# Kernel optimization log

Measured on AMD Instinct MI355X. Metric: run time of the kernel, lower is better.

The kernel has to match this reference:

```python
import jax, jax.numpy as jnp
import numpy as np

N_QUBITS = 4
N_LAYERS = 3
B = 262144

_H = (np.array([[1, 1], [1, -1]], np.complex64) / np.sqrt(2.0)).astype(np.complex64)
_X = np.array([[0, 1], [1, 0]], np.complex64)


def _rx(th):
    c = jnp.cos(th / 2); s = jnp.sin(th / 2)
    return jnp.stack([jnp.stack([c + 0j, -1j * s]), jnp.stack([-1j * s, c + 0j])]).astype(jnp.complex64)


def _ry(th):
    c = jnp.cos(th / 2); s = jnp.sin(th / 2)
    return jnp.stack([jnp.stack([c + 0j, -s + 0j]), jnp.stack([s + 0j, c + 0j])]).astype(jnp.complex64)


def _rz(th):
    e = jnp.exp(-0.5j * th.astype(jnp.complex64))
    z = jnp.zeros((), jnp.complex64)
    return jnp.stack([jnp.stack([e, z]), jnp.stack([z, jnp.conj(e)])])


def _ap1(psi, U, q):
    # shared 2x2 gate on qubit q; psi: (B,2,2,2,2)
    psi = jnp.moveaxis(psi, q + 1, -1)
    psi = jnp.einsum('ij,...j->...i', U, psi)
    return jnp.moveaxis(psi, -1, q + 1)


def _ap1b(psi, U, q):
    # per-sample 2x2 gate U:(B,2,2)
    psi = jnp.moveaxis(psi, q + 1, -1)
    psi = jnp.einsum('bij,b...j->b...i', U, psi)
    return jnp.moveaxis(psi, -1, q + 1)


def _apc(psi, U, c, t):
    # controlled-U, control qubit c, target t
    psi = jnp.moveaxis(psi, (c + 1, t + 1), (-2, -1))
    top = psi[..., 0, :]
    bot = jnp.einsum('ij,...j->...i', U, psi[..., 1, :])
    psi = jnp.stack([top, bot], axis=-2)
    return jnp.moveaxis(psi, (-2, -1), (c + 1, t + 1))


def _apmcx(psi, controls, t):
    # multi-controlled X (here Toffoli-like with 3 controls)
    src = tuple(c + 1 for c in controls) + (t + 1,)
    k = len(src)
    dst = tuple(range(-k, 0))
    psi = jnp.moveaxis(psi, src, dst)
    idx = (Ellipsis,) + (1,) * len(controls)
    psi = psi.at[idx].set(psi[idx][..., ::-1])
    return jnp.moveaxis(psi, dst, src)


def _qforward(x, weights, entangle_weights, gammas, betas):
    b = x.shape[0]
    psi = jnp.zeros((b, 2, 2, 2, 2), jnp.complex64).at[:, 0, 0, 0, 0].set(1.0)
    # AngleEmbedding with RY rotations (per-sample angles)
    for q in range(N_QUBITS):
        th = x[:, q]
        c, s = jnp.cos(th / 2), jnp.sin(th / 2)
        U = jnp.stack([jnp.stack([c, -s], -1), jnp.stack([s, c], -1)], -2).astype(jnp.complex64)
        psi = _ap1b(psi, U, q)
    for layer in range(N_LAYERS):
        # trainable RX,RY,RZ (same angle per qubit)
        for q in range(N_QUBITS):
            th = weights[layer, q]
            psi = _ap1(psi, _rx(th), q)
            psi = _ap1(psi, _ry(th), q)
            psi = _ap1(psi, _rz(th), q)
        # CRX ring entangler
        for i in range(N_QUBITS):
            psi = _apc(psi, _rx(entangle_weights[layer, i]), i, (i + 1) % N_QUBITS)
        # Grover diffusion
        for q in range(N_QUBITS):
            psi = _ap1(psi, _H, q)
        for q in range(N_QUBITS):
            psi = _ap1(psi, _X, q)
        psi = _ap1(psi, _H, N_QUBITS - 1)
        psi = _apmcx(psi, list(range(N_QUBITS - 1)), N_QUBITS - 1)
        psi = _ap1(psi, _H, N_QUBITS - 1)
        for q in range(N_QUBITS):
            psi = _ap1(psi, _X, q)
        for q in range(N_QUBITS):
            psi = _ap1(psi, _H, q)
        # QAOA cost + mixer
        g, bt = gammas[layer], betas[layer]
        Urz, Urx = _rz(g), _rx(bt)
        for i in range(N_QUBITS - 1):
            psi = _apc(psi, _X, i, i + 1)
            psi = _ap1(psi, Urz, i + 1)
            psi = _apc(psi, _X, i, i + 1)
        for q in range(N_QUBITS):
            psi = _ap1(psi, Urx, q)
    # multi-basis measurements: Z then X then Y on every qubit
    outs = {'z': [], 'x': [], 'y': []}
    for q in range(N_QUBITS):
        p = jnp.moveaxis(psi, q + 1, -1)  # (B, 2,2,2, 2)
        a, d = p[..., 0], p[..., 1]
        axes = tuple(range(1, N_QUBITS))
        outs['z'].append(jnp.sum(jnp.abs(a) ** 2 - jnp.abs(d) ** 2, axis=axes))
        cross = jnp.sum(jnp.conj(a) * d, axis=axes)
        outs['x'].append(2.0 * jnp.real(cross))
        outs['y'].append(2.0 * jnp.imag(cross))
    return jnp.stack(outs['z'] + outs['x'] + outs['y'], axis=1).astype(jnp.float32)


def setup_inputs() -> dict:
    key = jax.random.key(0)
    k0, k1, k2, k3, k4 = jax.random.split(key, 5)
    return {
        'x': jax.random.normal(k0, (B, N_QUBITS), jnp.float32),
        'weights': 0.01 * jax.random.normal(k1, (N_LAYERS, N_QUBITS), jnp.float32),
        'entangle_weights': 0.01 * jax.random.normal(k2, (N_LAYERS, N_QUBITS), jnp.float32),
        'gammas': 0.01 * jax.random.normal(k3, (N_LAYERS,), jnp.float32),
        'betas': 0.01 * jax.random.normal(k4, (N_LAYERS,), jnp.float32),
    }


def reference(x, weights, entangle_weights, gammas, betas):
    return _qforward(x, weights, entangle_weights, gammas, betas)
```

## Files before the change

kernel.cpp:

```cpp
#include <hip/hip_runtime.h>


#define RL(x, l) __int_as_float(__builtin_amdgcn_readlane(__float_as_int(x), (l)))


__device__ __forceinline__ void g_rx(float& ar, float& ai, int amp, int m,
                                     float c, float s, int cmask) {
    const float br = __shfl_xor(ar, 1 << m, 64);
    const float bi = __shfl_xor(ai, 1 << m, 64);
    const float nr = c * ar + s * bi;
    const float ni = c * ai - s * br;
    const bool act = (amp & cmask) == cmask;
    ar = act ? nr : ar;
    ai = act ? ni : ai;
}

__device__ __forceinline__ void g_ry(float& ar, float& ai, int amp, int m,
                                     float c, float s) {
    const float br = __shfl_xor(ar, 1 << m, 64);
    const float bi = __shfl_xor(ai, 1 << m, 64);
    const float sp = ((amp >> m) & 1) ? s : -s;
    ar = c * ar + sp * br;
    ai = c * ai + sp * bi;
}

__device__ __forceinline__ void g_rz(float& ar, float& ai, int amp, int m,
                                     float c, float s) {
    const float p = ((amp >> m) & 1) ? s : -s;
    const float nr = c * ar - p * ai;
    const float ni = c * ai + p * ar;
    ar = nr; ai = ni;
}

__device__ __forceinline__ void g_h(float& ar, float& ai, int amp, int m) {
    const float R = 0.70710678118654752440f;
    const float br = __shfl_xor(ar, 1 << m, 64);
    const float bi = __shfl_xor(ai, 1 << m, 64);
    const bool hi = (amp >> m) & 1;
    ar = hi ? R * (br - ar) : R * (ar + br);
    ai = hi ? R * (bi - ai) : R * (ai + bi);
}

__device__ __forceinline__ void g_swap(float& ar, float& ai, int m, bool act) {
    const float br = __shfl_xor(ar, 1 << m, 64);
    const float bi = __shfl_xor(ai, 1 << m, 64);
    ar = act ? br : ar;
    ai = act ? bi : ai;
}

__device__ __forceinline__ void emit_obs(const float* pr, const float* pi,
                                         float* __restrict__ out, int b) {
    float n[16];
#pragma unroll
    for (int i = 0; i < 16; ++i) n[i] = pr[i] * pr[i] + pi[i] * pi[i];
    float o[12];
#pragma unroll
    for (int q = 0; q < 4; ++q) {
        const int m = 3 - q;
        const int mask = 1 << m;
        float z = 0.f, cr = 0.f, ci = 0.f;
#pragma unroll
        for (int p = 0; p < 8; ++p) {
            const int i0 = ((p >> m) << (m + 1)) | (p & (mask - 1));
            const int i1 = i0 | mask;
            z  += n[i0] - n[i1];
            cr += pr[i0] * pr[i1] + pi[i0] * pi[i1];
            ci += pr[i0] * pi[i1] - pi[i0] * pr[i1];
        }
        o[q]     = z;
        o[4 + q] = 2.f * cr;
        o[8 + q] = 2.f * ci;
    }
    float4* op = reinterpret_cast<float4*>(out + (size_t)b * 12);
    op[0] = make_float4(o[0], o[1], o[2],  o[3]);
    op[1] = make_float4(o[4], o[5], o[6],  o[7]);
    op[2] = make_float4(o[8], o[9], o[10], o[11]);
}

__global__ __launch_bounds__(256)
void qnn_prep(const float* __restrict__ W,  const float* __restrict__ E,
              const float* __restrict__ G,  const float* __restrict__ Bt,
              float* __restrict__ Uout) {
    __shared__ float2 cs[30];

    const int tid = threadIdx.x;

    if (tid < 30) {
        float th;
        if (tid < 12)      th = W[tid];
        else if (tid < 24) th = E[tid - 12];
        else if (tid < 27) th = G[tid - 24];
        else               th = Bt[tid - 27];
        float s, c;
        __sincosf(0.5f * th, &s, &c);
        cs[tid] = make_float2(c, s);
    }
    __syncthreads();

    const int col = tid >> 4;
    const int amp = tid & 15;
    float ar = (amp == col) ? 1.f : 0.f;
    float ai = 0.f;

    for (int l = 0; l < 3; ++l) {
#pragma unroll
        for (int q = 0; q < 4; ++q) {
            const float2 cw = cs[l * 4 + q];
            g_rx(ar, ai, amp, 3 - q, cw.x, cw.y, 0);
            g_ry(ar, ai, amp, 3 - q, cw.x, cw.y);
            g_rz(ar, ai, amp, 3 - q, cw.x, cw.y);
        }
#pragma unroll
        for (int i = 0; i < 4; ++i) {
            const float2 ce = cs[12 + l * 4 + i];
            g_rx(ar, ai, amp, 3 - ((i + 1) & 3), ce.x, ce.y, 1 << (3 - i));
        }
#pragma unroll
        for (int q = 0; q < 4; ++q) g_h(ar, ai, amp, 3 - q);
#pragma unroll
        for (int q = 0; q < 4; ++q) g_swap(ar, ai, 3 - q, true);
        g_h(ar, ai, amp, 0);
        g_swap(ar, ai, 3, (amp & 7) == 7);
        g_h(ar, ai, amp, 0);
#pragma unroll
        for (int q = 0; q < 4; ++q) g_swap(ar, ai, 3 - q, true);
#pragma unroll
        for (int q = 0; q < 4; ++q) g_h(ar, ai, amp, 3 - q);
        {
            const float2 cg = cs[24 + l];
#pragma unroll
            for (int i = 0; i < 3; ++i) {
                const int cm = 1 << (3 - i);
                const int m  = 2 - i;
                g_swap(ar, ai, m, (amp & cm) == cm);
                g_rz(ar, ai, amp, m, cg.x, cg.y);
                g_swap(ar, ai, m, (amp & cm) == cm);
            }
        }
        {
            const float2 cb = cs[27 + l];
#pragma unroll
            for (int q = 0; q < 4; ++q) g_rx(ar, ai, amp, 3 - q, cb.x, cb.y, 0);
        }
    }

    Uout[amp * 32 + 2 * col]     = ar;
    Uout[amp * 32 + 2 * col + 1] = ai;
}

__global__ __launch_bounds__(256, 2)
void qnn_main(const float* __restrict__ x, const float* __restrict__ Uin,
              float* __restrict__ out, int half) {
    const int tid  = threadIdx.x;
    const int lane = tid & 63;

    const int b0 = blockIdx.x * 256 + tid;
    const int b1 = b0 + half;
    const float4 x0 = reinterpret_cast<const float4*>(x)[b0];
    const float4 x1 = reinterpret_cast<const float4*>(x)[b1];

    const float4 ua = reinterpret_cast<const float4*>(Uin)[2 * lane];
    const float4 ub = reinterpret_cast<const float4*>(Uin)[2 * lane + 1];
    const float u[8] = { ua.x, ua.y, ua.z, ua.w, ub.x, ub.y, ub.z, ub.w };

    float v0[16], v1[16];
    {
        float c0, s0, c1, s1, c2, s2, c3, s3;
        __sincosf(0.5f * x0.x, &s0, &c0);
        __sincosf(0.5f * x0.y, &s1, &c1);
        __sincosf(0.5f * x0.z, &s2, &c2);
        __sincosf(0.5f * x0.w, &s3, &c3);
        const float t01[4] = { c0 * c1, c0 * s1, s0 * c1, s0 * s1 };
        const float t23[4] = { c2 * c3, c2 * s3, s2 * c3, s2 * s3 };
#pragma unroll
        for (int i = 0; i < 16; ++i) v0[i] = t01[i >> 2] * t23[i & 3];
    }
    {
        float c0, s0, c1, s1, c2, s2, c3, s3;
        __sincosf(0.5f * x1.x, &s0, &c0);
        __sincosf(0.5f * x1.y, &s1, &c1);
        __sincosf(0.5f * x1.z, &s2, &c2);
        __sincosf(0.5f * x1.w, &s3, &c3);
        const float t01[4] = { c0 * c1, c0 * s1, s0 * c1, s0 * s1 };
        const float t23[4] = { c2 * c3, c2 * s3, s2 * c3, s2 * s3 };
#pragma unroll
        for (int i = 0; i < 16; ++i) v1[i] = t01[i >> 2] * t23[i & 3];
    }

    float pr0[16], pi0[16], pr1[16], pi1[16];
#pragma unroll
    for (int i = 0; i < 16; ++i) {
        float a0r = 0.f, a0i = 0.f, a1r = 0.f, a1i = 0.f;
#pragma unroll
        for (int j = 0; j < 16; ++j) {
            const int f = i * 32 + 2 * j;
            const float sUr = RL(u[f & 7], f >> 3);
            const float sUi = RL(u[(f & 7) + 1], f >> 3);
            a0r = fmaf(sUr, v0[j], a0r);
            a0i = fmaf(sUi, v0[j], a0i);
            a1r = fmaf(sUr, v1[j], a1r);
            a1i = fmaf(sUi, v1[j], a1i);
        }
        pr0[i] = a0r; pi0[i] = a0i;
        pr1[i] = a1r; pi1[i] = a1i;
    }

    emit_obs(pr0, pi0, out, b0);
    emit_obs(pr1, pi1, out, b1);
}

extern "C" void kernel_launch(void* const* d_in, const int* in_sizes, int n_in,
                              void* d_out, int out_size, void* d_ws, size_t ws_size,
                              hipStream_t stream) {
    const float* x  = (const float*)d_in[0];
    const float* W  = (const float*)d_in[1];
    const float* E  = (const float*)d_in[2];
    const float* G  = (const float*)d_in[3];
    const float* Bt = (const float*)d_in[4];
    float* out = (float*)d_out;
    float* Uws = (float*)d_ws;
    (void)ws_size; (void)n_in; (void)out_size;

    const int B = in_sizes[0] / 4;
    const int half = B / 2;
    const int blocks = half / 256;

    hipLaunchKernelGGL(qnn_prep, dim3(1), dim3(256), 0, stream,
                       W, E, G, Bt, Uws);
    hipLaunchKernelGGL(qnn_main, dim3(blocks), dim3(256), 0, stream,
                       x, Uws, out, half);
}
```

Before: 78.13 us.

## Build per-layer unitaries in parallel and combine them with matrix products

The single-block prep kernel now uses 768 threads, so each 256-thread group simulates one of the three layers at the same time instead of looping over the layers in sequence. The three 16x16 layer unitaries are written to shared memory and multiplied together (L2·L1·L0) to form the full circuit unitary. This shortens the serial prep kernel that runs before the main batch kernel. In exchange it adds two matrix-multiply phases with extra barriers, and the larger block may raise register pressure.

```diff
diff --git a/kernel.cpp b/kernel.cpp
--- a/kernel.cpp
+++ b/kernel.cpp
@@ -77,11 +77,13 @@
     op[2] = make_float4(o[8], o[9], o[10], o[11]);
 }
 
-__global__ __launch_bounds__(256)
+__global__ __launch_bounds__(768)
 void qnn_prep(const float* __restrict__ W,  const float* __restrict__ E,
               const float* __restrict__ G,  const float* __restrict__ Bt,
               float* __restrict__ Uout) {
     __shared__ float2 cs[30];
+    __shared__ float2 Lsh[3][256];
+    __shared__ float2 Msh[256];
 
     const int tid = threadIdx.x;
 
@@ -97,12 +99,15 @@
     }
     __syncthreads();
 
-    const int col = tid >> 4;
-    const int amp = tid & 15;
+    const int g   = tid >> 8;
+    const int t2  = tid & 255;
+    const int col = t2 >> 4;
+    const int amp = t2 & 15;
     float ar = (amp == col) ? 1.f : 0.f;
     float ai = 0.f;
 
-    for (int l = 0; l < 3; ++l) {
+    {
+        const int l = g;
 #pragma unroll
         for (int q = 0; q < 4; ++q) {
             const float2 cw = cs[l * 4 + q];
@@ -144,8 +149,36 @@
         }
     }
 
-    Uout[amp * 32 + 2 * col]     = ar;
-    Uout[amp * 32 + 2 * col + 1] = ai;
+    Lsh[g][amp * 16 + col] = make_float2(ar, ai);
+    __syncthreads();
+
+    const int i = t2 & 15;
+    const int j = t2 >> 4;
+    if (g == 0) {
+        float mr = 0.f, mi = 0.f;
+#pragma unroll
+        for (int k = 0; k < 16; ++k) {
+            const float2 a = Lsh[1][i * 16 + k];
+            const float2 b = Lsh[0][k * 16 + j];
+            mr = fmaf(a.x, b.x, fmaf(-a.y, b.y, mr));
+            mi = fmaf(a.x, b.y, fmaf( a.y, b.x, mi));
+        }
+        Msh[i * 16 + j] = make_float2(mr, mi);
+    }
+    __syncthreads();
+
+    if (g == 0) {
+        float ur = 0.f, ui = 0.f;
+#pragma unroll
+        for (int k = 0; k < 16; ++k) {
+            const float2 a = Lsh[2][i * 16 + k];
+            const float2 b = Msh[k * 16 + j];
+            ur = fmaf(a.x, b.x, fmaf(-a.y, b.y, ur));
+            ui = fmaf(a.x, b.y, fmaf( a.y, b.x, ui));
+        }
+        Uout[i * 32 + 2 * j]     = ur;
+        Uout[i * 32 + 2 * j + 1] = ui;
+    }
 }
 
 __global__ __launch_bounds__(256, 2)
@@ -225,7 +258,7 @@
     const int half = B / 2;
     const int blocks = half / 256;
 
-    hipLaunchKernelGGL(qnn_prep, dim3(1), dim3(256), 0, stream,
+    hipLaunchKernelGGL(qnn_prep, dim3(1), dim3(768), 0, stream,
                        W, E, G, Bt, Uws);
     hipLaunchKernelGGL(qnn_main, dim3(blocks), dim3(256), 0, stream,
                        x, Uws, out, half);
```

Result: no change. 78.21 us (+0.1%).
